# Kernel tuning notes

Hardware: AMD Instinct MI355X
Metric: run time of the kernel (lower is better)

## Reference

```python
import jax, jax.numpy as jnp
import numpy as np

N_NODES = 100000
N_GRAPHS = 512
EMB = 64
IN_FEAT = 12
N_EDGES = 3200000


def setup_inputs() -> dict:
    key = jax.random.key(0)
    ks = jax.random.split(key, 16)
    x = jax.random.normal(ks[0], (N_NODES, IN_FEAT), dtype=jnp.float32)
    edge_index = jax.random.randint(ks[1], (2, N_EDGES), 0, N_NODES, dtype=jnp.int64)
    batch_index = jnp.sort(jax.random.randint(ks[2], (N_NODES,), 0, N_GRAPHS, dtype=jnp.int64))

    def glorot(k, shape):
        lim = float(np.sqrt(6.0 / (shape[0] + shape[1])))
        return jax.random.uniform(k, shape, jnp.float32, -lim, lim)

    W0 = glorot(ks[3], (IN_FEAT, EMB)); b0 = jnp.zeros((EMB,), jnp.float32)
    W1 = glorot(ks[4], (EMB, EMB));     b1 = jnp.zeros((EMB,), jnp.float32)
    W2 = glorot(ks[5], (EMB, EMB));     b2 = jnp.zeros((EMB,), jnp.float32)
    W3 = glorot(ks[6], (EMB, EMB));     b3 = jnp.zeros((EMB,), jnp.float32)
    Wfc = glorot(ks[7], (EMB, 1));      bfc = jnp.zeros((1,), jnp.float32)
    return {"x": x, "edge_index": edge_index, "batch_index": batch_index,
            "W0": W0, "b0": b0, "W1": W1, "b1": b1, "W2": W2, "b2": b2,
            "W3": W3, "b3": b3, "Wfc": Wfc, "bfc": bfc}


def _gcn_conv(x, src, dst, norm, W, b):
    # x' = scatter_add(norm * (x W)[src] -> dst) + b   (self-loops already in src/dst)
    h = x @ W                              # [N, d_out]
    msg = h[src] * norm[:, None]           # [E+N, d_out] gather + normalize
    out = jax.ops.segment_sum(msg, dst, num_segments=x.shape[0])
    return out + b


def _gcn_forward(x, edge_index, batch_index, W0, b0, W1, b1, W2, b2, W3, b3, Wfc, bfc):
    N = x.shape[0]
    loop = jnp.arange(N, dtype=edge_index.dtype)
    src = jnp.concatenate([edge_index[0], loop])   # add self-loops
    dst = jnp.concatenate([edge_index[1], loop])
    deg = jax.ops.segment_sum(jnp.ones_like(dst, dtype=x.dtype), dst, num_segments=N)
    d_isqrt = jnp.where(deg > 0, jax.lax.rsqrt(deg), 0.0)
    norm = d_isqrt[src] * d_isqrt[dst]             # symmetric normalization

    h = jax.nn.leaky_relu(_gcn_conv(x, src, dst, norm, W0, b0), 0.01)
    h = jax.nn.leaky_relu(_gcn_conv(h, src, dst, norm, W1, b1), 0.01)
    h = jax.nn.leaky_relu(_gcn_conv(h, src, dst, norm, W2, b2), 0.01)
    h = jax.nn.relu(_gcn_conv(h, src, dst, norm, W3, b3))

    # global mean pool over graphs
    sums = jax.ops.segment_sum(h, batch_index, num_segments=N_GRAPHS)   # [G, EMB]
    cnts = jax.ops.segment_sum(jnp.ones((N,), h.dtype), batch_index, num_segments=N_GRAPHS)
    pooled = sums / jnp.maximum(cnts, 1.0)[:, None]

    return jax.nn.sigmoid(pooled @ Wfc + bfc)      # [G, 1]


def reference(x, edge_index, batch_index, W0, b0, W1, b1, W2, b2, W3, b3, Wfc, bfc):
    return _gcn_forward(x, edge_index, batch_index, W0, b0, W1, b1, W2, b2, W3, b3, Wfc, bfc)
```

## Files before the change

kernel.cpp:

```cpp
#include <hip/hip_runtime.h>
#include <math.h>

#define N_NODES 100000
#define N_GRAPHS 512
#define EMB 64
#define NBKT 196
#define BSH 9
#define CHUNK_E 4096

typedef unsigned int uint;
typedef __fp16 half_t;
typedef half_t h2_t __attribute__((ext_vector_type(2)));

__device__ __forceinline__ h2_t uint_as_h2(uint u) {
    union { uint u; h2_t h; } c; c.u = u; return c.h;
}
__device__ __forceinline__ uint h2_as_uint(h2_t h) {
    union { uint u; h2_t h; } c; c.h = h; return c.u;
}
__device__ __forceinline__ uint packh2(float a, float b) {
    return h2_as_uint(__builtin_amdgcn_cvt_pkrtz(a, b));
}

#if __has_builtin(__builtin_amdgcn_fdot2)
#define FDOT2(a, b, c) __builtin_amdgcn_fdot2((a), (b), (c), false)
#else
__device__ __forceinline__ float FDOT2(h2_t a, h2_t b, float c) {
    return c + (float)a[0] * (float)b[0] + (float)a[1] * (float)b[1];
}
#endif

__device__ __forceinline__ float bflo(uint u) { return __uint_as_float(u << 16); }
__device__ __forceinline__ float bfhi(uint u) { return __uint_as_float(u & 0xffff0000u); }
__device__ __forceinline__ uint rne16(float f) {
    uint u = __float_as_uint(f);
    return (u + 0x7fffu + ((u >> 16) & 1u)) >> 16;
}
__device__ __forceinline__ uint pack2(float a, float b) {
    return rne16(a) | (rne16(b) << 16);
}

__global__ void k_zero_f(float* __restrict__ p, int n) {
    int i = blockIdx.x * blockDim.x + threadIdx.x;
    int stride = gridDim.x * blockDim.x;
    for (; i < n; i += stride) p[i] = 0.0f;
}
__global__ void k_zero_i(int* __restrict__ p, int n) {
    int i = blockIdx.x * blockDim.x + threadIdx.x;
    int stride = gridDim.x * blockDim.x;
    for (; i < n; i += stride) p[i] = 0;
}

__global__ __launch_bounds__(256) void k_bhist(const int* __restrict__ dst, int E,
                                               int* __restrict__ bcnt) {
    __shared__ int w[NBKT];
    for (int i = threadIdx.x; i < NBKT; i += 256) w[i] = 0;
    __syncthreads();
    int i = blockIdx.x * 256 + threadIdx.x;
    int stride = gridDim.x * 256;
    for (; i < E; i += stride) atomicAdd(&w[dst[i] >> BSH], 1);
    __syncthreads();
    for (int t = threadIdx.x; t < NBKT; t += 256)
        if (w[t]) atomicAdd(&bcnt[t], w[t]);
}

__global__ void k_bscan(const int* __restrict__ bcnt, int* __restrict__ bstart,
                        int* __restrict__ bcursor) {
    if (blockIdx.x == 0 && threadIdx.x == 0) {
        int run = 0;
        for (int b = 0; b < NBKT; ++b) { bstart[b] = run; bcursor[b] = run; run += bcnt[b]; }
        bstart[NBKT] = run;
    }
}

__global__ __launch_bounds__(256) void k_bscatter(
    const int* __restrict__ src, const int* __restrict__ dst, int E,
    int* __restrict__ bcursor, int2* __restrict__ sp) {
    __shared__ int wcnt[NBKT];
    __shared__ int wbase[NBKT];
    __shared__ int lofs[NBKT];
    __shared__ int lcur[NBKT];
    __shared__ int2 stage[CHUNK_E];
    __shared__ short sbkt[CHUNK_E];

    int e0 = blockIdx.x * CHUNK_E;
    int e1 = e0 + CHUNK_E;
    if (e1 > E) e1 = E;
    int t = threadIdx.x;

    for (int i = t; i < NBKT; i += 256) { wcnt[i] = 0; lcur[i] = 0; }
    __syncthreads();
    for (int i = e0 + t; i < e1; i += 256) atomicAdd(&wcnt[dst[i] >> BSH], 1);
    __syncthreads();
    if (t < NBKT) wbase[t] = atomicAdd(&bcursor[t], wcnt[t]);
    if (t == 0) {
        int run = 0;
        for (int b = 0; b < NBKT; ++b) { lofs[b] = run; run += wcnt[b]; }
    }
    __syncthreads();
    for (int i = e0 + t; i < e1; i += 256) {
        int d = dst[i];
        int b = d >> BSH;
        int l = lofs[b] + atomicAdd(&lcur[b], 1);
        stage[l] = make_int2(src[i], d);
        sbkt[l] = (short)b;
    }
    __syncthreads();
    int n = e1 - e0;
    for (int k = t; k < n; k += 256) {
        int b = sbkt[k];
        sp[wbase[b] + (k - lofs[b])] = stage[k];
    }
}

__global__ __launch_bounds__(512) void k_csr(const int2* __restrict__ sp,
                                             const int* __restrict__ bstart,
                                             int* __restrict__ rowptr,
                                             float* __restrict__ dsq,
                                             int* __restrict__ csr) {
    __shared__ int lcnt[512];
    __shared__ int wsum[8];
    int b = blockIdx.x, base = b << BSH, t = threadIdx.x;
    lcnt[t] = 0;
    __syncthreads();
    int s0 = bstart[b], s1 = bstart[b + 1];
    for (int i = s0 + t; i < s1; i += 512) atomicAdd(&lcnt[sp[i].y - base], 1);
    __syncthreads();
    int c = lcnt[t];
    int lane = t & 63, wid = t >> 6;
    int inc = c;
    for (int off = 1; off < 64; off <<= 1) {
        int v = __shfl_up(inc, off, 64);
        if (lane >= off) inc += v;
    }
    if (lane == 63) wsum[wid] = inc;
    __syncthreads();
    int wbase = 0;
    for (int w = 0; w < wid; ++w) wbase += wsum[w];
    int p = s0 + wbase + inc - c;
    int n = base + t;
    lcnt[t] = p;
    if (n < N_NODES) { rowptr[n] = p; dsq[n] = rsqrtf((float)c + 1.0f); }
    if (b == NBKT - 1 && t == 511) rowptr[N_NODES] = s1;
    __syncthreads();
    for (int i = s0 + t; i < s1; i += 512) {
        int2 pr = sp[i];
        int pos = atomicAdd(&lcnt[pr.y - base], 1);
        csr[pos] = pr.x;
    }
}

__global__ void k_xprep2(const float* __restrict__ x, const float* __restrict__ dsq,
                         uint* __restrict__ xp2) {
    int i = blockIdx.x * blockDim.x + threadIdx.x;
    int stride = gridDim.x * blockDim.x;
    const int total = N_NODES * 8;
    for (; i < total; i += stride) {
        int n = i >> 3, u = i & 7;
        int c0 = 2 * u, c1 = c0 + 1;
        float d = dsq[n];
        float v0 = (c0 < 12) ? x[n * 12 + c0] * d : 0.0f;
        float v1 = (c1 < 12) ? x[n * 12 + c1] * d : 0.0f;
        xp2[i] = pack2(v0, v1);
    }
}

__device__ __forceinline__ void store_fp8_row(uint* __restrict__ hout, int node,
                                              int lane, float sv) {
    float pv = __shfl_xor(sv, 1, 64);
    uint w = (uint)__builtin_amdgcn_cvt_pk_fp8_f32(sv, pv, 0, false);
    uint w2 = __shfl_xor(w, 2, 64);
    if ((lane & 3) == 0) hout[node * 16 + (lane >> 2)] = (w & 0xffffu) | (w2 << 16);
}

template <int ACT, int LAST>
__global__ __launch_bounds__(256) void k_layer64f(
    const int* __restrict__ rowptr, const int* __restrict__ csr,
    const float* __restrict__ dsq, const uint2* __restrict__ hin,
    const float* __restrict__ W, const float* __restrict__ b,
    uint* __restrict__ hout, float* __restrict__ houtf) {
    __shared__ uint rowsh[4][32];

    int wid = threadIdx.x >> 6;
    int lane = threadIdx.x & 63;
    int q = lane >> 3;
    int cc = lane & 7;

    uint wreg[32];
#pragma unroll
    for (int m = 0; m < 32; ++m)
        wreg[m] = packh2(W[(2 * m) * 64 + lane], W[(2 * m + 1) * 64 + lane]);
    float bias = b[lane];

    for (int grp = blockIdx.x; grp < N_NODES / 4; grp += gridDim.x) {
        int node = grp * 4 + wid;
        int start = rowptr[node], end = rowptr[node + 1];
        float dn = dsq[node];

        float a0 = 0.0f, a1 = 0.0f, a2 = 0.0f, a3 = 0.0f;
        float a4 = 0.0f, a5 = 0.0f, a6 = 0.0f, a7 = 0.0f;
#define ACCU(u) do { \
        auto f0 = __builtin_amdgcn_cvt_pk_f32_fp8(u.x, false); \
        auto f1 = __builtin_amdgcn_cvt_pk_f32_fp8(u.x, true);  \
        auto f2 = __builtin_amdgcn_cvt_pk_f32_fp8(u.y, false); \
        auto f3 = __builtin_amdgcn_cvt_pk_f32_fp8(u.y, true);  \
        a0 += f0[0]; a1 += f0[1]; a2 += f1[0]; a3 += f1[1]; \
        a4 += f2[0]; a5 += f2[1]; a6 += f3[0]; a7 += f3[1]; } while (0)

        if (q == 0) {
            uint2 u = hin[node * 8 + cc];
            ACCU(u);
        }

        for (int k0 = start; k0 < end; k0 += 64) {
            int idx = k0 + lane;
            int s = (idx < end) ? csr[idx] : 0;
            int nk = end - k0; if (nk > 64) nk = 64;
            for (int jj = 0; jj < nk; jj += 32) {
                int e0 = jj + q, e1 = jj + 8 + q, e2 = jj + 16 + q, e3 = jj + 24 + q;
                int s0 = __shfl(s, e0, 64);
                int s1 = __shfl(s, e1, 64);
                int s2 = __shfl(s, e2, 64);
                int s3 = __shfl(s, e3, 64);
                uint2 u0 = make_uint2(0u, 0u), u1 = make_uint2(0u, 0u);
                uint2 u2 = make_uint2(0u, 0u), u3 = make_uint2(0u, 0u);
                if (e0 < nk) u0 = hin[s0 * 8 + cc];
                if (e1 < nk) u1 = hin[s1 * 8 + cc];
                if (e2 < nk) u2 = hin[s2 * 8 + cc];
                if (e3 < nk) u3 = hin[s3 * 8 + cc];
                ACCU(u0); ACCU(u1); ACCU(u2); ACCU(u3);
            }
        }
#undef ACCU
#define RED(a) a += __shfl_xor(a, 8, 64); a += __shfl_xor(a, 16, 64); a += __shfl_xor(a, 32, 64)
        RED(a0); RED(a1); RED(a2); RED(a3); RED(a4); RED(a5); RED(a6); RED(a7);
#undef RED
        if (q == 0) {
            float g = dn * (1.0f / 16.0f);
            uint4 pk;
            pk.x = packh2(g * a0, g * a1);
            pk.y = packh2(g * a2, g * a3);
            pk.z = packh2(g * a4, g * a5);
            pk.w = packh2(g * a6, g * a7);
            *(uint4*)&rowsh[wid][cc * 4] = pk;
        }

        float sacc = bias;
#pragma unroll
        for (int j = 0; j < 8; ++j) {
            uint4 r = *(const uint4*)&rowsh[wid][4 * j];
            sacc = FDOT2(uint_as_h2(r.x), uint_as_h2(wreg[4 * j + 0]), sacc);
            sacc = FDOT2(uint_as_h2(r.y), uint_as_h2(wreg[4 * j + 1]), sacc);
            sacc = FDOT2(uint_as_h2(r.z), uint_as_h2(wreg[4 * j + 2]), sacc);
            sacc = FDOT2(uint_as_h2(r.w), uint_as_h2(wreg[4 * j + 3]), sacc);
        }
        float val = ACT ? fmaxf(sacc, 0.0f) : (sacc > 0.0f ? sacc : 0.01f * sacc);

        if (LAST) {
            houtf[node * 64 + lane] = val;
        } else {
            store_fp8_row(hout, node, lane, 16.0f * dn * val);
        }
    }
}

__global__ __launch_bounds__(256) void k_layer12(
    const int* __restrict__ rowptr, const int* __restrict__ csr,
    const float* __restrict__ dsq, const uint2* __restrict__ xp2,
    const float* __restrict__ W, const float* __restrict__ b,
    uint* __restrict__ hout) {
    __shared__ float Wl[12 * 64];
    __shared__ float rows[4][16];
    for (int i = threadIdx.x; i < 12 * 64; i += 256) Wl[i] = W[i];

    int wid = threadIdx.x >> 6;
    int lane = threadIdx.x & 63;
    int node = blockIdx.x * 4 + wid;
    int q = lane >> 2;
    int cc = lane & 3;

    int start = rowptr[node], end = rowptr[node + 1];
    float dn = dsq[node];

    float a0 = 0.0f, a1 = 0.0f, a2 = 0.0f, a3 = 0.0f;
    if (q == 0) {
        uint2 u = xp2[node * 4 + cc];
        a0 = bflo(u.x); a1 = bfhi(u.x); a2 = bflo(u.y); a3 = bfhi(u.y);
    }

    for (int k0 = start; k0 < end; k0 += 64) {
        int idx = k0 + lane;
        int s = (idx < end) ? csr[idx] : 0;
        int nk = end - k0; if (nk > 64) nk = 64;
        for (int jj = 0; jj < nk; jj += 32) {
            int e0 = jj + q, e1 = jj + 16 + q;
            int s0 = __shfl(s, e0, 64);
            int s1 = __shfl(s, e1, 64);
            uint2 u0 = make_uint2(0u, 0u), u1 = make_uint2(0u, 0u);
            if (e0 < nk) u0 = xp2[s0 * 4 + cc];
            if (e1 < nk) u1 = xp2[s1 * 4 + cc];
            a0 += bflo(u0.x); a1 += bfhi(u0.x); a2 += bflo(u0.y); a3 += bfhi(u0.y);
            a0 += bflo(u1.x); a1 += bfhi(u1.x); a2 += bflo(u1.y); a3 += bfhi(u1.y);
        }
    }
    a0 += __shfl_xor(a0, 4, 64); a0 += __shfl_xor(a0, 8, 64);
    a0 += __shfl_xor(a0, 16, 64); a0 += __shfl_xor(a0, 32, 64);
    a1 += __shfl_xor(a1, 4, 64); a1 += __shfl_xor(a1, 8, 64);
    a1 += __shfl_xor(a1, 16, 64); a1 += __shfl_xor(a1, 32, 64);
    a2 += __shfl_xor(a2, 4, 64); a2 += __shfl_xor(a2, 8, 64);
    a2 += __shfl_xor(a2, 16, 64); a2 += __shfl_xor(a2, 32, 64);
    a3 += __shfl_xor(a3, 4, 64); a3 += __shfl_xor(a3, 8, 64);
    a3 += __shfl_xor(a3, 16, 64); a3 += __shfl_xor(a3, 32, 64);
    if (q == 0) {
        rows[wid][4 * cc + 0] = dn * a0;
        rows[wid][4 * cc + 1] = dn * a1;
        rows[wid][4 * cc + 2] = dn * a2;
        rows[wid][4 * cc + 3] = dn * a3;
    }
    __syncthreads();

    float sacc = b[lane];
#pragma unroll
    for (int k = 0; k < 12; ++k) sacc += rows[wid][k] * Wl[k * 64 + lane];
    float val = (sacc > 0.0f) ? sacc : 0.01f * sacc;
    store_fp8_row(hout, node, lane, 16.0f * dn * val);
}

__global__ void k_pool(const float* __restrict__ h, const int* __restrict__ batch,
                       float* __restrict__ psum, float* __restrict__ pcnt) {
    const int CHUNK = 256;
    int lane = threadIdx.x;
    int start = blockIdx.x * CHUNK;
    if (start >= N_NODES) return;
    int end = start + CHUNK;
    if (end > N_NODES) end = N_NODES;

    int curg = batch[start];
    float acc = 0.0f;
    int cnt = 0;
    for (int n = start; n < end; ++n) {
        int g = batch[n];
        if (g != curg) {
            atomicAdd(&psum[curg * EMB + lane], acc);
            if (lane == 0) atomicAdd(&pcnt[curg], (float)cnt);
            acc = 0.0f; cnt = 0; curg = g;
        }
        acc += h[n * EMB + lane];
        ++cnt;
    }
    atomicAdd(&psum[curg * EMB + lane], acc);
    if (lane == 0) atomicAdd(&pcnt[curg], (float)cnt);
}

__global__ void k_fc(const float* __restrict__ psum, const float* __restrict__ pcnt,
                     const float* __restrict__ Wfc, const float* __restrict__ bfc,
                     float* __restrict__ out) {
    int g = blockIdx.x;
    int lane = threadIdx.x;
    float v = psum[g * EMB + lane] * Wfc[lane];
#pragma unroll
    for (int off = 32; off; off >>= 1) v += __shfl_down(v, off, 64);
    if (lane == 0) {
        float c = fmaxf(pcnt[g], 1.0f);
        float z = v / c + bfc[0];
        out[g] = 1.0f / (1.0f + expf(-z));
    }
}

extern "C" void kernel_launch(void* const* d_in, const int* in_sizes, int n_in,
                              void* d_out, int out_size, void* d_ws, size_t ws_size,
                              hipStream_t stream) {
    const float* x     = (const float*)d_in[0];
    const int*   edge  = (const int*)d_in[1];
    const int*   batch = (const int*)d_in[2];
    const float* W0 = (const float*)d_in[3];
    const float* b0 = (const float*)d_in[4];
    const float* W1 = (const float*)d_in[5];
    const float* b1 = (const float*)d_in[6];
    const float* W2 = (const float*)d_in[7];
    const float* b2 = (const float*)d_in[8];
    const float* W3 = (const float*)d_in[9];
    const float* b3 = (const float*)d_in[10];
    const float* Wfc = (const float*)d_in[11];
    const float* bfc = (const float*)d_in[12];
    float* out = (float*)d_out;

    const int E = in_sizes[1] / 2;
    const int* src = edge;
    const int* dst = edge + E;

    char* ws = (char*)d_ws;
    float* dsq    = (float*)ws;                   ws += sizeof(float) * N_NODES;
    int*   rowptr = (int*)ws;                     ws += sizeof(int) * (N_NODES + 1);
    int*   bcnt   = (int*)ws;                     ws += sizeof(int) * 256;
    int*   bstart = (int*)ws;                     ws += sizeof(int) * 256;
    int*   bcursor= (int*)ws;                     ws += sizeof(int) * 256;
    ws = (char*)(((size_t)ws + 15) & ~(size_t)15);
    uint*  xp2    = (uint*)ws;                    ws += sizeof(uint) * N_NODES * 8;
    int*   csr    = (int*)ws;                     ws += sizeof(int) * E;
    uint*  bufA   = (uint*)ws;                    ws += sizeof(uint) * N_NODES * 16;
    uint*  bufB   = (uint*)ws;                    ws += sizeof(uint) * N_NODES * 16;
    float* bufF   = (float*)ws;                   ws += sizeof(float) * N_NODES * EMB;
    float* psum   = (float*)ws;                   ws += sizeof(float) * N_GRAPHS * EMB;
    float* pcnt   = (float*)ws;
    int2*  sp     = (int2*)bufF;

    k_zero_i<<<1, 256, 0, stream>>>(bcnt, 256);
    k_bhist<<<512, 256, 0, stream>>>(dst, E, bcnt);
    k_bscan<<<1, 64, 0, stream>>>(bcnt, bstart, bcursor);
    k_bscatter<<<(E + CHUNK_E - 1) / CHUNK_E, 256, 0, stream>>>(src, dst, E, bcursor, sp);
    k_csr<<<NBKT, 512, 0, stream>>>(sp, bstart, rowptr, dsq, csr);
    k_xprep2<<<512, 256, 0, stream>>>(x, dsq, xp2);

    const int NBLK = N_NODES / 4;
    k_layer12<<<NBLK, 256, 0, stream>>>(rowptr, csr, dsq, (const uint2*)xp2, W0, b0, bufA);
    k_layer64f<0, 0><<<4096, 256, 0, stream>>>(rowptr, csr, dsq, (const uint2*)bufA, W1, b1, bufB, nullptr);
    k_layer64f<0, 0><<<4096, 256, 0, stream>>>(rowptr, csr, dsq, (const uint2*)bufB, W2, b2, bufA, nullptr);
    k_layer64f<1, 1><<<4096, 256, 0, stream>>>(rowptr, csr, dsq, (const uint2*)bufA, W3, b3, nullptr, bufF);

    k_zero_f<<<64, 256, 0, stream>>>(psum, N_GRAPHS * EMB + N_GRAPHS);
    k_pool<<<(N_NODES + 255) / 256, 64, 0, stream>>>(bufF, batch, psum, pcnt);
    k_fc<<<N_GRAPHS, 64, 0, stream>>>(psum, pcnt, Wfc, bfc, out);
}
```

Baseline: 440.9 us.

## Fuse mean pool and FC head using precomputed graph boundaries

Computes per-graph start offsets from the sorted batch index in a small kernel, then replaces the zero/atomic pool/fc sequence with one kernel that has a block per graph. Each block sums its contiguous node range with float4 loads and applies the FC and sigmoid directly. This removes two launches, the global atomics and the psum round trip. The cost is an extra boundary kernel, and it relies on batch_index being sorted, which the spec guarantees.

```diff
diff --git a/kernel.cpp b/kernel.cpp
--- a/kernel.cpp
+++ b/kernel.cpp
@@ -40,11 +40,6 @@
     return rne16(a) | (rne16(b) << 16);
 }
 
-__global__ void k_zero_f(float* __restrict__ p, int n) {
-    int i = blockIdx.x * blockDim.x + threadIdx.x;
-    int stride = gridDim.x * blockDim.x;
-    for (; i < n; i += stride) p[i] = 0.0f;
-}
 __global__ void k_zero_i(int* __restrict__ p, int n) {
     int i = blockIdx.x * blockDim.x + threadIdx.x;
     int stride = gridDim.x * blockDim.x;
@@ -147,6 +142,21 @@
         int2 pr = sp[i];
         int pos = atomicAdd(&lcnt[pr.y - base], 1);
         csr[pos] = pr.x;
+    }
+}
+
+__global__ void k_gbound(const int* __restrict__ batch, int* __restrict__ gstart) {
+    int i = blockIdx.x * blockDim.x + threadIdx.x;
+    if (i >= N_NODES) return;
+    int b = batch[i];
+    if (i == 0) {
+        for (int g = 0; g <= b; ++g) gstart[g] = 0;
+    } else {
+        int pb = batch[i - 1];
+        for (int g = pb + 1; g <= b; ++g) gstart[g] = i;
+    }
+    if (i == N_NODES - 1) {
+        for (int g = b + 1; g <= N_GRAPHS; ++g) gstart[g] = N_NODES;
     }
 }
 
@@ -326,44 +336,43 @@
     store_fp8_row(hout, node, lane, 16.0f * dn * val);
 }
 
-__global__ void k_pool(const float* __restrict__ h, const int* __restrict__ batch,
-                       float* __restrict__ psum, float* __restrict__ pcnt) {
-    const int CHUNK = 256;
-    int lane = threadIdx.x;
-    int start = blockIdx.x * CHUNK;
-    if (start >= N_NODES) return;
-    int end = start + CHUNK;
-    if (end > N_NODES) end = N_NODES;
-
-    int curg = batch[start];
-    float acc = 0.0f;
-    int cnt = 0;
-    for (int n = start; n < end; ++n) {
-        int g = batch[n];
-        if (g != curg) {
-            atomicAdd(&psum[curg * EMB + lane], acc);
-            if (lane == 0) atomicAdd(&pcnt[curg], (float)cnt);
-            acc = 0.0f; cnt = 0; curg = g;
-        }
-        acc += h[n * EMB + lane];
-        ++cnt;
-    }
-    atomicAdd(&psum[curg * EMB + lane], acc);
-    if (lane == 0) atomicAdd(&pcnt[curg], (float)cnt);
-}
-
-__global__ void k_fc(const float* __restrict__ psum, const float* __restrict__ pcnt,
-                     const float* __restrict__ Wfc, const float* __restrict__ bfc,
-                     float* __restrict__ out) {
+__global__ __launch_bounds__(256) void k_poolfc(
+    const float* __restrict__ h, const int* __restrict__ gstart,
+    const float* __restrict__ Wfc, const float* __restrict__ bfc,
+    float* __restrict__ out) {
+    __shared__ float sums[4][64];
     int g = blockIdx.x;
-    int lane = threadIdx.x;
-    float v = psum[g * EMB + lane] * Wfc[lane];
+    int t = threadIdx.x;
+    int w = t >> 6, lane = t & 63;
+    int q = lane & 15, sub = lane >> 4;
+    int s0 = gstart[g], s1 = gstart[g + 1];
+
+    float a0 = 0.0f, a1 = 0.0f, a2 = 0.0f, a3 = 0.0f;
+    for (int n = s0 + w * 4 + sub; n < s1; n += 16) {
+        float4 v = *(const float4*)&h[n * 64 + q * 4];
+        a0 += v.x; a1 += v.y; a2 += v.z; a3 += v.w;
+    }
+    a0 += __shfl_xor(a0, 16, 64); a0 += __shfl_xor(a0, 32, 64);
+    a1 += __shfl_xor(a1, 16, 64); a1 += __shfl_xor(a1, 32, 64);
+    a2 += __shfl_xor(a2, 16, 64); a2 += __shfl_xor(a2, 32, 64);
+    a3 += __shfl_xor(a3, 16, 64); a3 += __shfl_xor(a3, 32, 64);
+    if (lane < 16) {
+        sums[w][4 * lane + 0] = a0;
+        sums[w][4 * lane + 1] = a1;
+        sums[w][4 * lane + 2] = a2;
+        sums[w][4 * lane + 3] = a3;
+    }
+    __syncthreads();
+    if (t < 64) {
+        float tot = sums[0][t] + sums[1][t] + sums[2][t] + sums[3][t];
+        float v = tot * Wfc[t];
 #pragma unroll
-    for (int off = 32; off; off >>= 1) v += __shfl_down(v, off, 64);
-    if (lane == 0) {
-        float c = fmaxf(pcnt[g], 1.0f);
-        float z = v / c + bfc[0];
-        out[g] = 1.0f / (1.0f + expf(-z));
+        for (int off = 32; off; off >>= 1) v += __shfl_down(v, off, 64);
+        if (t == 0) {
+            float cnt = fmaxf((float)(s1 - s0), 1.0f);
+            float z = v / cnt + bfc[0];
+            out[g] = 1.0f / (1.0f + expf(-z));
+        }
     }
 }
 
@@ -395,14 +404,13 @@
     int*   bcnt   = (int*)ws;                     ws += sizeof(int) * 256;
     int*   bstart = (int*)ws;                     ws += sizeof(int) * 256;
     int*   bcursor= (int*)ws;                     ws += sizeof(int) * 256;
+    int*   gstart = (int*)ws;                     ws += sizeof(int) * (N_GRAPHS + 1);
     ws = (char*)(((size_t)ws + 15) & ~(size_t)15);
     uint*  xp2    = (uint*)ws;                    ws += sizeof(uint) * N_NODES * 8;
     int*   csr    = (int*)ws;                     ws += sizeof(int) * E;
     uint*  bufA   = (uint*)ws;                    ws += sizeof(uint) * N_NODES * 16;
     uint*  bufB   = (uint*)ws;                    ws += sizeof(uint) * N_NODES * 16;
     float* bufF   = (float*)ws;                   ws += sizeof(float) * N_NODES * EMB;
-    float* psum   = (float*)ws;                   ws += sizeof(float) * N_GRAPHS * EMB;
-    float* pcnt   = (float*)ws;
     int2*  sp     = (int2*)bufF;
 
     k_zero_i<<<1, 256, 0, stream>>>(bcnt, 256);
@@ -410,6 +418,7 @@
     k_bscan<<<1, 64, 0, stream>>>(bcnt, bstart, bcursor);
     k_bscatter<<<(E + CHUNK_E - 1) / CHUNK_E, 256, 0, stream>>>(src, dst, E, bcursor, sp);
     k_csr<<<NBKT, 512, 0, stream>>>(sp, bstart, rowptr, dsq, csr);
+    k_gbound<<<(N_NODES + 255) / 256, 256, 0, stream>>>(batch, gstart);
     k_xprep2<<<512, 256, 0, stream>>>(x, dsq, xp2);
 
     const int NBLK = N_NODES / 4;
@@ -418,7 +427,5 @@
     k_layer64f<0, 0><<<4096, 256, 0, stream>>>(rowptr, csr, dsq, (const uint2*)bufB, W2, b2, bufA, nullptr);
     k_layer64f<1, 1><<<4096, 256, 0, stream>>>(rowptr, csr, dsq, (const uint2*)bufA, W3, b3, nullptr, bufF);
 
-    k_zero_f<<<64, 256, 0, stream>>>(psum, N_GRAPHS * EMB + N_GRAPHS);
-    k_pool<<<(N_NODES + 255) / 256, 64, 0, stream>>>(bufF, batch, psum, pcnt);
-    k_fc<<<N_GRAPHS, 64, 0, stream>>>(psum, pcnt, Wfc, bfc, out);
-}
+    k_poolfc<<<N_GRAPHS, 256, 0, stream>>>(bufF, gstart, Wfc, bfc, out);
+}
```

New measurement: 374.5 us. -15.1%, faster.
